# Kernel optimization log

Hardware: AMD Instinct MI355X
Metric: run time of the kernel (lower is better)

## Reference

```python
import jax, jax.numpy as jnp
import numpy as np

BINS = 8

def setup_inputs() -> dict:
    key = jax.random.key(0)
    k1, k2, k3 = jax.random.split(key, 3)
    B, H, W = 32, 160, 160
    HW = H * W
    reg_logits = jax.random.normal(k1, (B, 4 * BINS, H, W), dtype=jnp.float32)
    targets = jax.random.uniform(k2, (B, HW, 4), dtype=jnp.float32) * (BINS - 1)
    pos_mask = jax.random.randint(k3, (B, HW), 0, 2) == 1
    return {"reg_logits": reg_logits, "targets": targets, "pos_mask": pos_mask}

def reference(reg_logits, targets, pos_mask):
    bins = BINS
    B, C, H, W = reg_logits.shape
    HW = H * W
    # [B, C, H, W] -> [B, HW, 4, bins]
    rl = reg_logits.transpose(0, 2, 3, 1).reshape(B, HW, 4, bins)
    t = jnp.clip(targets, 0.0, bins - 1 - 0.0001)          # [B, HW, 4]
    l_id = jnp.floor(t).astype(jnp.int32)
    u_id = jnp.minimum(l_id + 1, bins - 1)
    w_u = t - l_id.astype(t.dtype)
    w_l = 1.0 - w_u
    logp = jax.nn.log_softmax(rl, axis=-1)                 # [B, HW, 4, bins]
    nll_l = -jnp.take_along_axis(logp, l_id[..., None], axis=-1)[..., 0]
    nll_u = -jnp.take_along_axis(logp, u_id[..., None], axis=-1)[..., 0]
    per = w_l * nll_l + w_u * nll_u                        # [B, HW, 4]
    m = pos_mask.astype(per.dtype)                         # [B, HW]
    npos = jnp.sum(m)
    # mean over positives per coordinate, averaged over 4 coords ==
    # sum over (positives x 4) / (npos * 4)
    total = jnp.sum(per * m[..., None])
    loss = total / (jnp.maximum(npos, 1.0) * 4.0)
    return jnp.where(npos > 0, loss, jnp.zeros((), dtype=per.dtype))
```

## Files before the change

kernel.cpp:

```cpp
#include <hip/hip_runtime.h>

#define BINS 8
#define BLOCK 256

constexpr int BATCH   = 32;
constexpr int HW      = 25600;
constexpr int NPIX    = BATCH * HW;
constexpr int NGROUPS = NPIX / 4;
constexpr int NBLOCKS = NGROUPS / BLOCK;

__device__ __forceinline__ float comp4(const float4& v, int i) {
    return (i == 0) ? v.x : (i == 1) ? v.y : (i == 2) ? v.z : v.w;
}

__global__ __launch_bounds__(BLOCK) void dfl_main_kernel(
    const float* __restrict__ logits,
    const float* __restrict__ targets,
    const int*   __restrict__ mask,
    float* __restrict__ partials) {

    const int g  = blockIdx.x * BLOCK + threadIdx.x;
    const int p4 = g << 2;
    const int b  = p4 / HW;
    const int pp = p4 - b * HW;

    const float* base = logits + (size_t)b * 4 * BINS * HW + pp;

    const float4* tgt = (const float4*)(targets + (size_t)p4 * 4);
    float4 t4[4];
#pragma unroll
    for (int i = 0; i < 4; ++i) t4[i] = tgt[i];

    const int4 mk = *(const int4*)(mask + p4);
    float msk[4];
    msk[0] = mk.x ? 1.0f : 0.0f;
    msk[1] = mk.y ? 1.0f : 0.0f;
    msk[2] = mk.z ? 1.0f : 0.0f;
    msk[3] = mk.w ? 1.0f : 0.0f;

    float tsum = 0.0f;
    float tcnt = msk[0] + msk[1] + msk[2] + msk[3];

#pragma unroll
    for (int c = 0; c < 4; ++c) {
        float4 xv[BINS];
#pragma unroll
        for (int j = 0; j < BINS; ++j)
            xv[j] = *(const float4*)(base + (size_t)(c * BINS + j) * HW);

#pragma unroll
        for (int i = 0; i < 4; ++i) {
            float x[BINS];
#pragma unroll
            for (int j = 0; j < BINS; ++j) x[j] = comp4(xv[j], i);

            float t = comp4(t4[i], c);
            t = fminf(fmaxf(t, 0.0f), (float)(BINS - 1) - 0.0001f);
            float lf = floorf(t);
            int   li = (int)lf;
            int   ui = li + 1;
            float wu = t - lf;
            float wl = 1.0f - wu;

            float s = 0.0f;
#pragma unroll
            for (int j = 0; j < BINS; ++j) s += __expf(x[j]);
            float lse = __logf(s);

            float xl = x[0], xu = x[0];
#pragma unroll
            for (int j = 1; j < BINS; ++j) {
                xl = (li == j) ? x[j] : xl;
                xu = (ui == j) ? x[j] : xu;
            }

            tsum += msk[i] * (lse - (wl * xl + wu * xu));
        }
    }

#pragma unroll
    for (int off = 32; off > 0; off >>= 1) {
        tsum += __shfl_down(tsum, off, 64);
        tcnt += __shfl_down(tcnt, off, 64);
    }

    __shared__ float ssum[BLOCK / 64];
    __shared__ float scnt[BLOCK / 64];
    const int wid  = threadIdx.x >> 6;
    const int lane = threadIdx.x & 63;
    if (lane == 0) { ssum[wid] = tsum; scnt[wid] = tcnt; }
    __syncthreads();
    if (threadIdx.x == 0) {
        float bs = 0.0f, bc = 0.0f;
#pragma unroll
        for (int w = 0; w < BLOCK / 64; ++w) { bs += ssum[w]; bc += scnt[w]; }
        partials[2 * blockIdx.x]     = bs;
        partials[2 * blockIdx.x + 1] = bc;
    }
}

__global__ __launch_bounds__(BLOCK) void finalize_kernel(
    const float* __restrict__ partials, float* __restrict__ out) {

    float tsum = 0.0f, tcnt = 0.0f;
    for (int i = threadIdx.x; i < NBLOCKS; i += BLOCK) {
        tsum += partials[2 * i];
        tcnt += partials[2 * i + 1];
    }
#pragma unroll
    for (int off = 32; off > 0; off >>= 1) {
        tsum += __shfl_down(tsum, off, 64);
        tcnt += __shfl_down(tcnt, off, 64);
    }
    __shared__ float ssum[BLOCK / 64];
    __shared__ float scnt[BLOCK / 64];
    const int wid  = threadIdx.x >> 6;
    const int lane = threadIdx.x & 63;
    if (lane == 0) { ssum[wid] = tsum; scnt[wid] = tcnt; }
    __syncthreads();
    if (threadIdx.x == 0) {
        float total = 0.0f, npos = 0.0f;
#pragma unroll
        for (int w = 0; w < BLOCK / 64; ++w) { total += ssum[w]; npos += scnt[w]; }
        float loss = total / (fmaxf(npos, 1.0f) * 4.0f);
        out[0] = (npos > 0.0f) ? loss : 0.0f;
    }
}

extern "C" void kernel_launch(void* const* d_in, const int* in_sizes, int n_in,
                              void* d_out, int out_size, void* d_ws, size_t ws_size,
                              hipStream_t stream) {
    const float* logits  = (const float*)d_in[0];
    const float* targets = (const float*)d_in[1];
    const int*   mask    = (const int*)d_in[2];
    float* out      = (float*)d_out;
    float* partials = (float*)d_ws;

    dfl_main_kernel<<<NBLOCKS, BLOCK, 0, stream>>>(logits, targets, mask, partials);
    finalize_kernel<<<1, BLOCK, 0, stream>>>(partials, out);
}
```

Baseline: 172.7 us.

## Split coordinates across wavefronts so each thread handles one coordinate

Each block now covers 64 pixel-groups, and its four wavefronts each take one of the four box coordinates, where before every thread looped over all four. Each thread loads only 8 float4 logits instead of 32, which cuts register pressure, and the launch bounds ask for higher occupancy. The grid grows to four times as many blocks, mask loads are repeated per wavefront, and target reads become strided scalar loads. Because the mask count is now summed four times, the finalize step divides by the count directly instead of multiplying it by four.

After: 167.6 us. 3.0% less time.

```diff
diff --git a/kernel.cpp b/kernel.cpp
--- a/kernel.cpp
+++ b/kernel.cpp
@@ -7,29 +7,37 @@
 constexpr int HW      = 25600;
 constexpr int NPIX    = BATCH * HW;
 constexpr int NGROUPS = NPIX / 4;
-constexpr int NBLOCKS = NGROUPS / BLOCK;
+constexpr int GPB     = 64;
+constexpr int NBLOCKS = NGROUPS / GPB;
 
 __device__ __forceinline__ float comp4(const float4& v, int i) {
     return (i == 0) ? v.x : (i == 1) ? v.y : (i == 2) ? v.z : v.w;
 }
 
-__global__ __launch_bounds__(BLOCK) void dfl_main_kernel(
+__global__ __launch_bounds__(BLOCK, 8) void dfl_main_kernel(
     const float* __restrict__ logits,
     const float* __restrict__ targets,
     const int*   __restrict__ mask,
     float* __restrict__ partials) {
 
-    const int g  = blockIdx.x * BLOCK + threadIdx.x;
-    const int p4 = g << 2;
-    const int b  = p4 / HW;
-    const int pp = p4 - b * HW;
+    const int lane = threadIdx.x & 63;
+    const int c    = threadIdx.x >> 6;
+    const int g    = blockIdx.x * GPB + lane;
+    const int p4   = g << 2;
+    const int b    = p4 / HW;
+    const int pp   = p4 - b * HW;
 
-    const float* base = logits + (size_t)b * 4 * BINS * HW + pp;
+    const float* base = logits + ((size_t)b * 4 * BINS + (size_t)c * BINS) * HW + pp;
 
-    const float4* tgt = (const float4*)(targets + (size_t)p4 * 4);
-    float4 t4[4];
+    float4 xv[BINS];
 #pragma unroll
-    for (int i = 0; i < 4; ++i) t4[i] = tgt[i];
+    for (int j = 0; j < BINS; ++j)
+        xv[j] = *(const float4*)(base + (size_t)j * HW);
+
+    float tc[4];
+#pragma unroll
+    for (int i = 0; i < 4; ++i)
+        tc[i] = targets[(size_t)(p4 + i) * 4 + c];
 
     const int4 mk = *(const int4*)(mask + p4);
     float msk[4];
@@ -42,40 +50,26 @@
     float tcnt = msk[0] + msk[1] + msk[2] + msk[3];
 
 #pragma unroll
-    for (int c = 0; c < 4; ++c) {
-        float4 xv[BINS];
+    for (int i = 0; i < 4; ++i) {
+        float t = fminf(fmaxf(tc[i], 0.0f), (float)(BINS - 1) - 0.0001f);
+        float lf = floorf(t);
+        int   li = (int)lf;
+        float wu = t - lf;
+        float wl = 1.0f - wu;
+
+        float s = 0.0f;
 #pragma unroll
-        for (int j = 0; j < BINS; ++j)
-            xv[j] = *(const float4*)(base + (size_t)(c * BINS + j) * HW);
+        for (int j = 0; j < BINS; ++j) s += __expf(comp4(xv[j], i));
+        float lse = __logf(s);
 
+        float xl = comp4(xv[0], i);
+        float xu = comp4(xv[1], i);
 #pragma unroll
-        for (int i = 0; i < 4; ++i) {
-            float x[BINS];
+        for (int j = 1; j < BINS; ++j) xl = (li == j)     ? comp4(xv[j], i) : xl;
 #pragma unroll
-            for (int j = 0; j < BINS; ++j) x[j] = comp4(xv[j], i);
+        for (int j = 2; j < BINS; ++j) xu = (li == j - 1) ? comp4(xv[j], i) : xu;
 
-            float t = comp4(t4[i], c);
-            t = fminf(fmaxf(t, 0.0f), (float)(BINS - 1) - 0.0001f);
-            float lf = floorf(t);
-            int   li = (int)lf;
-            int   ui = li + 1;
-            float wu = t - lf;
-            float wl = 1.0f - wu;
-
-            float s = 0.0f;
-#pragma unroll
-            for (int j = 0; j < BINS; ++j) s += __expf(x[j]);
-            float lse = __logf(s);
-
-            float xl = x[0], xu = x[0];
-#pragma unroll
-            for (int j = 1; j < BINS; ++j) {
-                xl = (li == j) ? x[j] : xl;
-                xu = (ui == j) ? x[j] : xu;
-            }
-
-            tsum += msk[i] * (lse - (wl * xl + wu * xu));
-        }
+        tsum += msk[i] * (lse - (wl * xl + wu * xu));
     }
 
 #pragma unroll
@@ -86,9 +80,7 @@
 
     __shared__ float ssum[BLOCK / 64];
     __shared__ float scnt[BLOCK / 64];
-    const int wid  = threadIdx.x >> 6;
-    const int lane = threadIdx.x & 63;
-    if (lane == 0) { ssum[wid] = tsum; scnt[wid] = tcnt; }
+    if (lane == 0) { ssum[c] = tsum; scnt[c] = tcnt; }
     __syncthreads();
     if (threadIdx.x == 0) {
         float bs = 0.0f, bc = 0.0f;
@@ -119,11 +111,11 @@
     if (lane == 0) { ssum[wid] = tsum; scnt[wid] = tcnt; }
     __syncthreads();
     if (threadIdx.x == 0) {
-        float total = 0.0f, npos = 0.0f;
+        float total = 0.0f, npos4 = 0.0f;
 #pragma unroll
-        for (int w = 0; w < BLOCK / 64; ++w) { total += ssum[w]; npos += scnt[w]; }
-        float loss = total / (fmaxf(npos, 1.0f) * 4.0f);
-        out[0] = (npos > 0.0f) ? loss : 0.0f;
+        for (int w = 0; w < BLOCK / 64; ++w) { total += ssum[w]; npos4 += scnt[w]; }
+        float loss = total / fmaxf(npos4, 1.0f);
+        out[0] = (npos4 > 0.0f) ? loss : 0.0f;
     }
 }
 
```
